# Optimization experiments

Hardware: AMD Instinct MI355X
Metric: run time of the kernel (lower is better)

Reference implementation:

```python
import jax, jax.numpy as jnp
import numpy as np

B, L, D, C = 8, 1024, 512, 4  # batch, maxlen, input_units(=output_unit), channel


def setup_inputs() -> dict:
    key = jax.random.key(0)
    ks = jax.random.split(key, 6)
    scale = 1.0 / np.sqrt(D)  # glorot-ish
    inputs = jax.random.normal(ks[0], (B, L, D), dtype=jnp.float32)
    pad_k = jnp.zeros((B, L, 1), dtype=jnp.float32)  # 0 = valid, -99999 = pad
    w_l = jax.random.normal(ks[1], (C, D, D), dtype=jnp.float32) * scale   # scalar_w per channel
    b_l = jnp.zeros((C,), dtype=jnp.float32)                                # scalar_b per channel
    w_v1 = jax.random.normal(ks[2], (C, D), dtype=jnp.float32) * scale     # vector_w1 [D,1] squeezed
    w_v2 = jax.random.normal(ks[3], (C, D, D), dtype=jnp.float32) * scale  # vector_w2
    b_v = jnp.zeros((C, D), dtype=jnp.float32)                              # vector_b [1,1,D] squeezed
    return {"inputs": inputs, "pad_k": pad_k, "w_l": w_l, "b_l": b_l,
            "w_v1": w_v1, "w_v2": w_v2, "b_v": b_v}


def reference(inputs, pad_k, w_l, b_l, w_v1, w_v2, b_v):
    # inputs: [B,L,D], pad_k: [B,L,1]. Dropout (mask_prob) is identity at inference.
    pad_k2 = (pad_k + 99999.0) / 99999.0              # [B,L,1], 1 at valid, 0 at pad
    pk = pad_k[:, None, :, 0]                          # [B,1,L]

    # --- scalar (pairwise bilinear) attention, all channels at once ---
    mat_l = jnp.einsum('bld,cde->bcle', inputs, w_l)   # [B,C,L,D]
    # M[b,c,i,j] = sum_d inputs[b,i,d] * mat_l[b,c,j,d] + b_l[c]
    M = jnp.einsum('bid,bcjd->bcij', inputs, mat_l) + b_l[None, :, None, None]
    A = jnp.tanh(M)                                    # [B,C,L,L]
    s = A.sum(axis=3)                                  # sum over j -> [B,C,L]
    a = jax.nn.softmax(pk + s, axis=-1)[..., None]     # softmax over L -> [B,C,L,1]

    # --- vector attention ---
    sb = jnp.tanh(jnp.einsum('bld,cde->bcle', inputs, w_v2) + b_v[None, :, None, :])  # [B,C,L,D]
    score_bar = jnp.einsum('bcld,cd->bcl', sb, w_v1) + pk                              # [B,C,L]
    a_bar = jax.nn.softmax(score_bar, axis=-1)                                         # [B,C,L]
    pooled = jnp.einsum('bcl,bld->bcd', a_bar, inputs)                                 # [B,C,D]

    # C_l = a_l * inputs + pooled(broadcast over L) * pad_k2
    C_l = a * inputs[:, None] + pooled[:, :, None, :] * pad_k2[:, None]                # [B,C,L,D]

    C_features = jnp.concatenate(
        [jnp.transpose(C_l, (0, 2, 3, 1)), inputs[..., None]], axis=-1)                # [B,L,D,C+1]
    return C_features, a, a_bar[..., None]
```

## Files before the change

kernel.cpp:

```cpp
#include <hip/hip_runtime.h>

#define BB 8
#define LL 1024
#define DD 512
#define CC 4

typedef unsigned short u16;
typedef unsigned int u32;
typedef __attribute__((ext_vector_type(8))) short bf16x8;
typedef __attribute__((ext_vector_type(4))) float f32x4;
typedef __attribute__((ext_vector_type(4))) unsigned short u16x4;
typedef __attribute__((ext_vector_type(4))) float float4v;

typedef __attribute__((address_space(1))) const u32 gu32;
typedef __attribute__((address_space(3))) u32 lu32;
typedef __attribute__((address_space(3))) u16 l16;

__device__ __forceinline__ void gload16(const void* g, void* l) {
  __builtin_amdgcn_global_load_lds((gu32*)g, (lu32*)l, 16, 0, 0);
}
__device__ __forceinline__ u32 lds_off(const u16* p) {
  return (u32)(uintptr_t)(l16*)p;
}

__device__ __forceinline__ u16 f2bf(float f) {
  unsigned u = __float_as_uint(f);
  u += 0x7FFF + ((u >> 16) & 1);
  return (u16)(u >> 16);
}
__device__ __forceinline__ float bf2f(u16 h) {
  return __uint_as_float(((unsigned)h) << 16);
}
__device__ __forceinline__ float fast_tanh(float x) {
  return 1.0f - 2.0f / (__expf(2.0f * x) + 1.0f);
}

__global__ __launch_bounds__(256) void k_split(const float4v* __restrict__ x,
                                               u16* __restrict__ hi, u16* __restrict__ lo) {
  int i = blockIdx.x * 256 + threadIdx.x;
  float4v v = x[i];
  u16x4 h, l;
#pragma unroll
  for (int k = 0; k < 4; ++k) {
    u16 hh = f2bf(v[k]);
    h[k] = hh;
    l[k] = f2bf(v[k] - bf2f(hh));
  }
  *(u16x4*)&hi[(size_t)i * 4] = h;
  *(u16x4*)&lo[(size_t)i * 4] = l;
}

__global__ __launch_bounds__(256) void k_tsplit(const float* __restrict__ w,
                                                u16* __restrict__ thi, u16* __restrict__ tlo) {
  __shared__ float t[32][33];
  int c = blockIdx.z;
  int tx = threadIdx.x;
  int ty = threadIdx.y;
  int e0 = blockIdx.x * 32, d0 = blockIdx.y * 32;
#pragma unroll
  for (int k = 0; k < 32; k += 8)
    t[ty + k][tx] = w[((size_t)c * DD + d0 + ty + k) * DD + e0 + tx];
  __syncthreads();
#pragma unroll
  for (int k = 0; k < 32; k += 8) {
    float v = t[tx][ty + k];
    size_t o = ((size_t)c * DD + e0 + ty + k) * DD + d0 + tx;
    u16 h = f2bf(v);
    thi[o] = h;
    if (tlo) tlo[o] = f2bf(v - bf2f(h));
  }
}

#define DSR(dst, addr, OFF) \
  asm volatile("ds_read_b128 %0, %1 offset:" #OFF : "=v"(dst) : "v"(addr))
#define LGKM(N) \
  do { __builtin_amdgcn_sched_barrier(0); \
       asm volatile("s_waitcnt lgkmcnt(" #N ")" ::: "memory"); \
       __builtin_amdgcn_sched_barrier(0); } while (0)

template<int NSEG, bool SPLIT>
__device__ __forceinline__ void gemm256(const u16* __restrict__ Ahi, const u16* __restrict__ Alo,
                                        const u16* __restrict__ Bhi, const u16* __restrict__ Blo,
                                        u16* lA, u16* lB, f32x4 (&acc)[8][4]) {
  const int tid = threadIdx.x;
  const int lane = tid & 63;
  const int wave = tid >> 6;
  const int wr = wave >> 2, wc = wave & 3;
  const int fr = lane & 15;
  const int fq = lane >> 4;
  const int xs = (tid & 7) ^ ((tid >> 3) & 7);
  const size_t soff = (size_t)(tid >> 3) * DD + (size_t)xs * 8;
  const int p0 = fq ^ (fr & 7);
  const int dk = ((p0 ^ 4) - p0) * 16;
  const u32 ra = lds_off(lA) + (u32)((wr * 128 + fr) * 128 + p0 * 16);
  const u32 rb = lds_off(lB) + (u32)((wc * 64 + fr) * 128 + p0 * 16);

  const int NT = NSEG * 8;

#define STAGE_TOP(T, beo) do {                                                \
    const int seg_ = SPLIT ? ((T) >> 3) : 0;                                  \
    const int kp_ = ((T) & 7) * 64;                                           \
    const u16* As_ = (SPLIT && seg_ == 1) ? Alo : Ahi;                        \
    const u16* Bs_ = (SPLIT && seg_ == 2) ? Blo : Bhi;                        \
    gload16(As_ + soff + kp_,                 lA + (beo) + tid * 8);          \
    gload16(Bs_ + soff + kp_,                 lB + (beo) + tid * 8);          \
    gload16(As_ + soff + (size_t)64 * DD + kp_, lA + (beo) + tid * 8 + 4096); \
    gload16(Bs_ + soff + (size_t)64 * DD + kp_, lB + (beo) + tid * 8 + 4096); \
  } while (0)

#define STAGE_MID(T, beo) do {                                                \
    const int seg_ = SPLIT ? ((T) >> 3) : 0;                                  \
    const int kp_ = ((T) & 7) * 64;                                           \
    const u16* As_ = (SPLIT && seg_ == 1) ? Alo : Ahi;                        \
    const u16* Bs_ = (SPLIT && seg_ == 2) ? Blo : Bhi;                        \
    gload16(As_ + soff + (size_t)128 * DD + kp_, lA + (beo) + tid * 8 + 8192);  \
    gload16(Bs_ + soff + (size_t)128 * DD + kp_, lB + (beo) + tid * 8 + 8192);  \
    gload16(As_ + soff + (size_t)192 * DD + kp_, lA + (beo) + tid * 8 + 12288); \
    gload16(Bs_ + soff + (size_t)192 * DD + kp_, lB + (beo) + tid * 8 + 12288); \
  } while (0)

#define MFMA2(m0, m1) do {                                                    \
    _Pragma("unroll")                                                         \
    for (int ni = 0; ni < 4; ++ni)                                            \
      acc[m0][ni] = __builtin_amdgcn_mfma_f32_16x16x32_bf16(                  \
          af[m0], bv[ni], acc[m0][ni], 0, 0, 0);                              \
    _Pragma("unroll")                                                         \
    for (int ni = 0; ni < 4; ++ni)                                            \
      acc[m1][ni] = __builtin_amdgcn_mfma_f32_16x16x32_bf16(                  \
          af[m1], bv[ni], acc[m1][ni], 0, 0, 0);                              \
  } while (0)

#define HALF(aA_, aB_) do {                                                   \
    bf16x8 af[8], bv[4];                                                      \
    DSR(bv[0], aB_, 0);    DSR(bv[1], aB_, 2048);                             \
    DSR(bv[2], aB_, 4096); DSR(bv[3], aB_, 6144);                             \
    DSR(af[0], aA_, 0);    DSR(af[1], aA_, 2048);                             \
    DSR(af[2], aA_, 4096); DSR(af[3], aA_, 6144);                             \
    LGKM(2);                                                                  \
    MFMA2(0, 1);                                                              \
    DSR(af[4], aA_, 8192); DSR(af[5], aA_, 10240);                            \
    LGKM(2);                                                                  \
    MFMA2(2, 3);                                                              \
    DSR(af[6], aA_, 12288); DSR(af[7], aA_, 14336);                           \
    LGKM(2);                                                                  \
    MFMA2(4, 5);                                                              \
    LGKM(0);                                                                  \
    MFMA2(6, 7);                                                              \
  } while (0)

#define HALF_MID(aA_, aB_, T, beo) do {                                       \
    bf16x8 af[8], bv[4];                                                      \
    DSR(bv[0], aB_, 0);    DSR(bv[1], aB_, 2048);                             \
    DSR(bv[2], aB_, 4096); DSR(bv[3], aB_, 6144);                             \
    DSR(af[0], aA_, 0);    DSR(af[1], aA_, 2048);                             \
    DSR(af[2], aA_, 4096); DSR(af[3], aA_, 6144);                             \
    LGKM(2);                                                                  \
    MFMA2(0, 1);                                                              \
    DSR(af[4], aA_, 8192); DSR(af[5], aA_, 10240);                            \
    LGKM(2);                                                                  \
    MFMA2(2, 3);                                                              \
    STAGE_MID(T, beo);                                                        \
    DSR(af[6], aA_, 12288); DSR(af[7], aA_, 14336);                           \
    LGKM(2);                                                                  \
    MFMA2(4, 5);                                                              \
    LGKM(0);                                                                  \
    MFMA2(6, 7);                                                              \
  } while (0)

  STAGE_TOP(0, 0);
  STAGE_MID(0, 0);
  int beN = 16384;
  u32 bo = 0;
#pragma unroll 1
  for (int t = 0; t < NT - 1; ++t) {
    __builtin_amdgcn_sched_barrier(0);
    asm volatile("s_waitcnt vmcnt(0)" ::: "memory");
    __builtin_amdgcn_sched_barrier(0);
    __builtin_amdgcn_s_barrier();
    __builtin_amdgcn_sched_barrier(0);
    STAGE_TOP(t + 1, beN);
    {
      u32 aA0 = ra + bo, aB0 = rb + bo;
      __builtin_amdgcn_s_setprio(1);
      HALF_MID(aA0, aB0, t + 1, beN);
      u32 aA1 = aA0 + dk, aB1 = aB0 + dk;
      HALF(aA1, aB1);
      __builtin_amdgcn_s_setprio(0);
    }
    beN ^= 16384;
    bo ^= 32768u;
  }
  __builtin_amdgcn_sched_barrier(0);
  asm volatile("s_waitcnt vmcnt(0)" ::: "memory");
  __builtin_amdgcn_sched_barrier(0);
  __builtin_amdgcn_s_barrier();
  __builtin_amdgcn_sched_barrier(0);
  {
    u32 aA0 = ra + bo, aB0 = rb + bo;
    __builtin_amdgcn_s_setprio(1);
    HALF(aA0, aB0);
    u32 aA1 = aA0 + dk, aB1 = aB0 + dk;
    HALF(aA1, aB1);
    __builtin_amdgcn_s_setprio(0);
  }
#undef STAGE_TOP
#undef STAGE_MID
#undef HALF
#undef HALF_MID
#undef MFMA2
}

__global__ __launch_bounds__(512, 2) void k_matl(const u16* __restrict__ Xhi, const u16* __restrict__ Xlo,
                                                 const u16* __restrict__ Whi, const u16* __restrict__ Wlo,
                                                 u16* __restrict__ mhi, u16* __restrict__ mlo) {
  __shared__ u16 lA[2 * 256 * 64];
  __shared__ u16 lB[2 * 256 * 64];
  int lin = blockIdx.x;
  int virt = (lin & 7) * 32 + (lin >> 3);
  int bc = virt >> 3, rem = virt & 7;
  int tm = rem >> 1, tn = rem & 1;
  int b = bc >> 2, c = bc & 3;
  const u16* Ahi = Xhi + (size_t)b * LL * DD + (size_t)tm * 256 * DD;
  const u16* Alo = Xlo + (size_t)b * LL * DD + (size_t)tm * 256 * DD;
  const u16* Bhi = Whi + (size_t)c * DD * DD + (size_t)tn * 256 * DD;
  const u16* Blo = Wlo + (size_t)c * DD * DD + (size_t)tn * 256 * DD;
  f32x4 acc[8][4];
#pragma unroll
  for (int mi = 0; mi < 8; ++mi)
#pragma unroll
    for (int ni = 0; ni < 4; ++ni) acc[mi][ni] = (f32x4){0.f, 0.f, 0.f, 0.f};
  gemm256<3, true>(Ahi, Alo, Bhi, Blo, lA, lB, acc);

  int lane = threadIdx.x & 63, wave = threadIdx.x >> 6;
  int wr = wave >> 2, wc = wave & 3;
  int rgrp = (lane >> 4) * 4, cidx = lane & 15;
#pragma unroll
  for (int mi = 0; mi < 8; ++mi)
#pragma unroll
    for (int ni = 0; ni < 4; ++ni) {
      int row = tm * 256 + wr * 128 + mi * 16 + rgrp;
      int col = tn * 256 + wc * 64 + ni * 16 + cidx;
#pragma unroll
      for (int j = 0; j < 4; ++j) {
        float v = acc[mi][ni][j];
        size_t o = ((size_t)bc * LL + row + j) * DD + col;
        u16 h = f2bf(v);
        mhi[o] = h;
        mlo[o] = f2bf(v - bf2f(h));
      }
    }
}

__global__ __launch_bounds__(512, 2) void k_s(const u16* __restrict__ Xhi, const u16* __restrict__ Xlo,
                                              const u16* __restrict__ mhi, const u16* __restrict__ mlo,
                                              const float* __restrict__ b_l, float* __restrict__ s_part) {
  __shared__ u16 lA[2 * 256 * 64];
  __shared__ u16 lB[2 * 256 * 64];
  int lin = blockIdx.x;
  int virt = (lin & 7) * 64 + (lin >> 3);
  int bc = virt >> 4, rem = virt & 15;
  int tm = rem >> 2, tn = rem & 3;
  int b = bc >> 2, c = bc & 3;
  const u16* Ahi = Xhi + (size_t)b * LL * DD + (size_t)tm * 256 * DD;
  const u16* Alo = Xlo + (size_t)b * LL * DD + (size_t)tm * 256 * DD;
  const u16* Bhi = mhi + (size_t)bc * LL * DD + (size_t)tn * 256 * DD;
  const u16* Blo = mlo + (size_t)bc * LL * DD + (size_t)tn * 256 * DD;
  f32x4 acc[8][4];
#pragma unroll
  for (int mi = 0; mi < 8; ++mi)
#pragma unroll
    for (int ni = 0; ni < 4; ++ni) acc[mi][ni] = (f32x4){0.f, 0.f, 0.f, 0.f};
  gemm256<3, true>(Ahi, Alo, Bhi, Blo, lA, lB, acc);

  int lane = threadIdx.x & 63, wave = threadIdx.x >> 6;
  int wr = wave >> 2, wc = wave & 3;
  float bl = b_l[c];
  float part[8][4];
#pragma unroll
  for (int mi = 0; mi < 8; ++mi)
#pragma unroll
    for (int j = 0; j < 4; ++j) part[mi][j] = 0.f;
#pragma unroll
  for (int mi = 0; mi < 8; ++mi)
#pragma unroll
    for (int ni = 0; ni < 4; ++ni)
#pragma unroll
      for (int j = 0; j < 4; ++j) part[mi][j] += fast_tanh(acc[mi][ni][j] + bl);
#pragma unroll
  for (int mi = 0; mi < 8; ++mi)
#pragma unroll
    for (int j = 0; j < 4; ++j) {
      float v = part[mi][j];
      v += __shfl_xor(v, 1, 64);
      v += __shfl_xor(v, 2, 64);
      v += __shfl_xor(v, 4, 64);
      v += __shfl_xor(v, 8, 64);
      part[mi][j] = v;
    }
  if ((lane & 15) == 0) {
    int slot = bc * 16 + tn * 4 + wc;
    int rg = (lane >> 4) * 4;
#pragma unroll
    for (int mi = 0; mi < 8; ++mi)
#pragma unroll
      for (int j = 0; j < 4; ++j) {
        int row = tm * 256 + wr * 128 + mi * 16 + rg + j;
        s_part[(size_t)slot * LL + row] = part[mi][j];
      }
  }
}

__global__ __launch_bounds__(512, 2) void k_sbar(const u16* __restrict__ Xhi, const u16* __restrict__ Wv2T,
                                                 const float* __restrict__ b_v, const float* __restrict__ w_v1,
                                                 float* __restrict__ sc_part) {
  __shared__ u16 lA[2 * 256 * 64];
  __shared__ u16 lB[2 * 256 * 64];
  int lin = blockIdx.x;
  int virt = (lin & 7) * 32 + (lin >> 3);
  int bc = virt >> 3, rem = virt & 7;
  int tm = rem >> 1, tn = rem & 1;
  int b = bc >> 2, c = bc & 3;
  const u16* Ahi = Xhi + (size_t)b * LL * DD + (size_t)tm * 256 * DD;
  const u16* Bhi = Wv2T + (size_t)c * DD * DD + (size_t)tn * 256 * DD;
  f32x4 acc[8][4];
#pragma unroll
  for (int mi = 0; mi < 8; ++mi)
#pragma unroll
    for (int ni = 0; ni < 4; ++ni) acc[mi][ni] = (f32x4){0.f, 0.f, 0.f, 0.f};
  gemm256<1, false>(Ahi, nullptr, Bhi, nullptr, lA, lB, acc);

  int lane = threadIdx.x & 63, wave = threadIdx.x >> 6;
  int wr = wave >> 2, wc = wave & 3;
  int cidx = lane & 15;
  float wv[4], bvv[4];
#pragma unroll
  for (int ni = 0; ni < 4; ++ni) {
    int col = tn * 256 + wc * 64 + ni * 16 + cidx;
    wv[ni] = w_v1[c * DD + col];
    bvv[ni] = b_v[c * DD + col];
  }
  float part[8][4];
#pragma unroll
  for (int mi = 0; mi < 8; ++mi)
#pragma unroll
    for (int j = 0; j < 4; ++j) part[mi][j] = 0.f;
#pragma unroll
  for (int mi = 0; mi < 8; ++mi)
#pragma unroll
    for (int ni = 0; ni < 4; ++ni)
#pragma unroll
      for (int j = 0; j < 4; ++j) part[mi][j] += fast_tanh(acc[mi][ni][j] + bvv[ni]) * wv[ni];
#pragma unroll
  for (int mi = 0; mi < 8; ++mi)
#pragma unroll
    for (int j = 0; j < 4; ++j) {
      float v = part[mi][j];
      v += __shfl_xor(v, 1, 64);
      v += __shfl_xor(v, 2, 64);
      v += __shfl_xor(v, 4, 64);
      v += __shfl_xor(v, 8, 64);
      part[mi][j] = v;
    }
  if ((lane & 15) == 0) {
    int slot = bc * 8 + tn * 4 + wc;
    int rg = (lane >> 4) * 4;
#pragma unroll
    for (int mi = 0; mi < 8; ++mi)
#pragma unroll
      for (int j = 0; j < 4; ++j) {
        int row = tm * 256 + wr * 128 + mi * 16 + rg + j;
        sc_part[(size_t)slot * LL + row] = part[mi][j];
      }
  }
}

__device__ __forceinline__ float blk_max(float v, float* red, int tid) {
#pragma unroll
  for (int m = 32; m >= 1; m >>= 1) v = fmaxf(v, __shfl_xor(v, m, 64));
  if ((tid & 63) == 0) red[tid >> 6] = v;
  __syncthreads();
  float r = red[0];
#pragma unroll
  for (int k = 1; k < 16; ++k) r = fmaxf(r, red[k]);
  __syncthreads();
  return r;
}
__device__ __forceinline__ float blk_sum(float v, float* red, int tid) {
#pragma unroll
  for (int m = 32; m >= 1; m >>= 1) v += __shfl_xor(v, m, 64);
  if ((tid & 63) == 0) red[tid >> 6] = v;
  __syncthreads();
  float r = red[0];
#pragma unroll
  for (int k = 1; k < 16; ++k) r += red[k];
  __syncthreads();
  return r;
}

__global__ __launch_bounds__(1024) void k_softmax(const float* __restrict__ s_part,
                                                  const float* __restrict__ sc_part,
                                                  const float* __restrict__ pad_k,
                                                  const float* __restrict__ X,
                                                  float* __restrict__ a_out,
                                                  float* __restrict__ abar_out,
                                                  float* __restrict__ pooled) {
  __shared__ float red[16];
  __shared__ float sm_abar[LL];
  __shared__ float pp[DD];
  int bc = blockIdx.x, b = bc >> 2;
  int i = threadIdx.x;
  float pk = pad_k[b * LL + i];

  float s = pk;
#pragma unroll
  for (int p = 0; p < 16; ++p) s += s_part[(size_t)(bc * 16 + p) * LL + i];
  float mx = blk_max(s, red, i);
  float e = expf(s - mx);
  float sum = blk_sum(e, red, i);
  float a = e / sum;
  a_out[bc * LL + i] = a;

  float sb = pk;
#pragma unroll
  for (int p = 0; p < 8; ++p) sb += sc_part[(size_t)(bc * 8 + p) * LL + i];
  float mx2 = blk_max(sb, red, i);
  float e2 = expf(sb - mx2);
  float sum2 = blk_sum(e2, red, i);
  float ab = e2 / sum2;
  abar_out[bc * LL + i] = ab;
  sm_abar[i] = ab;
  __syncthreads();

  {
    int d = i & (DD - 1), h = i >> 9;
    const float* xb = X + (size_t)b * LL * DD + (size_t)h * 512 * DD + d;
    const float* abp = sm_abar + h * 512;
    float a0 = 0.f, a1 = 0.f, a2 = 0.f, a3 = 0.f;
    for (int l = 0; l < 512; l += 4) {
      a0 += abp[l + 0] * xb[(size_t)(l + 0) * DD];
      a1 += abp[l + 1] * xb[(size_t)(l + 1) * DD];
      a2 += abp[l + 2] * xb[(size_t)(l + 2) * DD];
      a3 += abp[l + 3] * xb[(size_t)(l + 3) * DD];
    }
    float sv = (a0 + a1) + (a2 + a3);
    if (h == 1) pp[d] = sv;
    __syncthreads();
    if (h == 0) pooled[bc * DD + d] = sv + pp[d];
  }
}

__global__ __launch_bounds__(256) void k_assemble(const float* __restrict__ X,
                                                  const float* __restrict__ pad_k,
                                                  const float* __restrict__ a,
                                                  const float* __restrict__ pooled,
                                                  float* __restrict__ out) {
  __shared__ float buf[1280];
  int t = threadIdx.x;
  size_t idx = (size_t)blockIdx.x * 256 + t;
  int d = (int)(idx & (DD - 1));
  int bl = (int)(idx >> 9);
  int b = bl >> 10;
  int l = bl & (LL - 1);
  float x = X[idx];
  float pk2 = (pad_k[bl] + 99999.0f) * (1.0f / 99999.0f);
#pragma unroll
  for (int c = 0; c < 4; ++c) {
    float av = a[(size_t)(b * 4 + c) * LL + l];
    float pv = pooled[(size_t)(b * 4 + c) * DD + d];
    buf[t * 5 + c] = av * x + pv * pk2;
  }
  buf[t * 5 + 4] = x;
  __syncthreads();
  size_t base = (size_t)blockIdx.x * 1280;
#pragma unroll
  for (int k = 0; k < 5; ++k) out[base + k * 256 + t] = buf[k * 256 + t];
}

extern "C" void kernel_launch(void* const* d_in, const int* in_sizes, int n_in,
                              void* d_out, int out_size, void* d_ws, size_t ws_size,
                              hipStream_t stream) {
  (void)in_sizes; (void)n_in; (void)out_size;
  const float* X     = (const float*)d_in[0];
  const float* pad_k = (const float*)d_in[1];
  const float* w_l   = (const float*)d_in[2];
  const float* b_l   = (const float*)d_in[3];
  const float* w_v1  = (const float*)d_in[4];
  const float* w_v2  = (const float*)d_in[5];
  const float* b_v   = (const float*)d_in[6];
  float* out = (float*)d_out;

  char* wsp = (char*)d_ws;
  const size_t NEED = 26279936;
  bool small_ws = ws_size < NEED;
  u16* Xhi = (u16*)wsp;
  u16* Xlo = small_ws ? (u16*)((char*)d_out + 67108864)
                      : (u16*)(wsp + 8388608);
  size_t off = small_ws ? 8388608 : 16777216;
  u16* WlThi = (u16*)(wsp + off);  off += 2097152;
  u16* WlTlo = (u16*)(wsp + off);  off += 2097152;
  u16* Wv2T  = (u16*)(wsp + off);  off += 2097152;
  float* s_part  = (float*)(wsp + off); off += 2097152;
  float* sc_part = (float*)(wsp + off); off += 1048576;
  float* pooled  = (float*)(wsp + off); off += 65536;

  u16* mhi = (u16*)d_out;
  u16* mlo = (u16*)d_out + 16777216;

  float* a_out    = out + 20971520;
  float* abar_out = out + 21004288;

  k_split<<<4096, 256, 0, stream>>>((const float4v*)X, Xhi, Xlo);
  k_tsplit<<<dim3(16, 16, 4), dim3(32, 8), 0, stream>>>(w_l, WlThi, WlTlo);
  k_tsplit<<<dim3(16, 16, 4), dim3(32, 8), 0, stream>>>(w_v2, Wv2T, nullptr);

  k_matl<<<256, 512, 0, stream>>>(Xhi, Xlo, WlThi, WlTlo, mhi, mlo);
  k_s<<<512, 512, 0, stream>>>(Xhi, Xlo, mhi, mlo, b_l, s_part);
  k_sbar<<<256, 512, 0, stream>>>(Xhi, Wv2T, b_v, w_v1, sc_part);

  k_softmax<<<32, 1024, 0, stream>>>(s_part, sc_part, pad_k, X, a_out, abar_out, pooled);
  k_assemble<<<16384, 256, 0, stream>>>(X, pad_k, a_out, pooled, out);
}
```

Before: 227.1 us.

## Split vector-pool out of softmax into parallel partial-sum and reduction kernels

Moves the a_bar-weighted pooling over L out of the 32-block softmax kernel into a 256-block kernel. Each block computes partial sums for all four channels over a 32-row chunk, so X is read once for all channels instead of once per channel. A second small kernel reduces the partials. This adds two launches and a 2MB workspace buffer in exchange for much higher parallelism in the pooling.

```diff
diff --git a/kernel.cpp b/kernel.cpp
--- a/kernel.cpp
+++ b/kernel.cpp
@@ -400,13 +400,9 @@
 __global__ __launch_bounds__(1024) void k_softmax(const float* __restrict__ s_part,
                                                   const float* __restrict__ sc_part,
                                                   const float* __restrict__ pad_k,
-                                                  const float* __restrict__ X,
                                                   float* __restrict__ a_out,
-                                                  float* __restrict__ abar_out,
-                                                  float* __restrict__ pooled) {
+                                                  float* __restrict__ abar_out) {
   __shared__ float red[16];
-  __shared__ float sm_abar[LL];
-  __shared__ float pp[DD];
   int bc = blockIdx.x, b = bc >> 2;
   int i = threadIdx.x;
   float pk = pad_k[b * LL + i];
@@ -417,8 +413,7 @@
   float mx = blk_max(s, red, i);
   float e = expf(s - mx);
   float sum = blk_sum(e, red, i);
-  float a = e / sum;
-  a_out[bc * LL + i] = a;
+  a_out[bc * LL + i] = e / sum;
 
   float sb = pk;
 #pragma unroll
@@ -426,27 +421,48 @@
   float mx2 = blk_max(sb, red, i);
   float e2 = expf(sb - mx2);
   float sum2 = blk_sum(e2, red, i);
-  float ab = e2 / sum2;
-  abar_out[bc * LL + i] = ab;
-  sm_abar[i] = ab;
-  __syncthreads();
-
-  {
-    int d = i & (DD - 1), h = i >> 9;
-    const float* xb = X + (size_t)b * LL * DD + (size_t)h * 512 * DD + d;
-    const float* abp = sm_abar + h * 512;
-    float a0 = 0.f, a1 = 0.f, a2 = 0.f, a3 = 0.f;
-    for (int l = 0; l < 512; l += 4) {
-      a0 += abp[l + 0] * xb[(size_t)(l + 0) * DD];
-      a1 += abp[l + 1] * xb[(size_t)(l + 1) * DD];
-      a2 += abp[l + 2] * xb[(size_t)(l + 2) * DD];
-      a3 += abp[l + 3] * xb[(size_t)(l + 3) * DD];
+  abar_out[bc * LL + i] = e2 / sum2;
+}
+
+__global__ __launch_bounds__(256) void k_pool2(const float* __restrict__ abar,
+                                               const float* __restrict__ X,
+                                               float* __restrict__ ppool) {
+  __shared__ float w[4][32];
+  int blk = blockIdx.x;
+  int b = blk >> 5, ch = blk & 31;
+  int t = threadIdx.x;
+  if (t < 128)
+    w[t >> 5][t & 31] = abar[(size_t)(b * 4 + (t >> 5)) * LL + ch * 32 + (t & 31)];
+  __syncthreads();
+  const float* xb = X + (size_t)b * LL * DD + (size_t)ch * 32 * DD;
+  float a0[4] = {0.f, 0.f, 0.f, 0.f}, a1[4] = {0.f, 0.f, 0.f, 0.f};
+  for (int j = 0; j < 32; ++j) {
+    float x0 = xb[(size_t)j * DD + t];
+    float x1 = xb[(size_t)j * DD + t + 256];
+#pragma unroll
+    for (int c = 0; c < 4; ++c) {
+      float wv = w[c][j];
+      a0[c] += wv * x0;
+      a1[c] += wv * x1;
     }
-    float sv = (a0 + a1) + (a2 + a3);
-    if (h == 1) pp[d] = sv;
-    __syncthreads();
-    if (h == 0) pooled[bc * DD + d] = sv + pp[d];
-  }
+  }
+  size_t base = (size_t)blk * 4 * DD;
+#pragma unroll
+  for (int c = 0; c < 4; ++c) {
+    ppool[base + c * DD + t] = a0[c];
+    ppool[base + c * DD + t + 256] = a1[c];
+  }
+}
+
+__global__ __launch_bounds__(512) void k_poolred(const float* __restrict__ ppool,
+                                                 float* __restrict__ pooled) {
+  int bc = blockIdx.x, b = bc >> 2, c = bc & 3;
+  int d = threadIdx.x;
+  float s = 0.f;
+#pragma unroll 4
+  for (int ch = 0; ch < 32; ++ch)
+    s += ppool[((size_t)(b * 32 + ch) * 4 + c) * DD + d];
+  pooled[bc * DD + d] = s;
 }
 
 __global__ __launch_bounds__(256) void k_assemble(const float* __restrict__ X,
@@ -490,7 +506,7 @@
   float* out = (float*)d_out;
 
   char* wsp = (char*)d_ws;
-  const size_t NEED = 26279936;
+  const size_t NEED = 28377088;
   bool small_ws = ws_size < NEED;
   u16* Xhi = (u16*)wsp;
   u16* Xlo = small_ws ? (u16*)((char*)d_out + 67108864)
@@ -502,6 +518,7 @@
   float* s_part  = (float*)(wsp + off); off += 2097152;
   float* sc_part = (float*)(wsp + off); off += 1048576;
   float* pooled  = (float*)(wsp + off); off += 65536;
+  float* ppool   = (float*)(wsp + off); off += 2097152;
 
   u16* mhi = (u16*)d_out;
   u16* mlo = (u16*)d_out + 16777216;
@@ -517,6 +534,8 @@
   k_s<<<512, 512, 0, stream>>>(Xhi, Xlo, mhi, mlo, b_l, s_part);
   k_sbar<<<256, 512, 0, stream>>>(Xhi, Wv2T, b_v, w_v1, sc_part);
 
-  k_softmax<<<32, 1024, 0, stream>>>(s_part, sc_part, pad_k, X, a_out, abar_out, pooled);
+  k_softmax<<<32, 1024, 0, stream>>>(s_part, sc_part, pad_k, a_out, abar_out);
+  k_pool2<<<256, 256, 0, stream>>>(abar_out, X, ppool);
+  k_poolred<<<32, 512, 0, stream>>>(ppool, pooled);
   k_assemble<<<16384, 256, 0, stream>>>(X, pad_k, a_out, pooled, out);
 }
```

New measurement: 214.2 us. 1.06x faster.
